# Performance work log

Hardware: AMD Instinct MI355X
Metric: run time of the kernel (lower is better)

The kernel has to match this reference:

```python
import jax, jax.numpy as jnp
import numpy as np

ALPHA = 0.2  # LeakyReLU negative slope
NUM_HEADS, OUT_DIM = 8, 16
N_NODES, N_EDGES, IN_DIM = 50000, 800000, 128


def setup_inputs() -> dict:
    key = jax.random.key(0)
    k = jax.random.split(key, 6)
    return {
        "x": jax.random.normal(k[0], (N_NODES, IN_DIM), dtype=jnp.float32),
        "W1": jax.random.normal(k[1], (IN_DIM, IN_DIM), dtype=jnp.float32) * (1.414 / np.sqrt(IN_DIM)),
        "W2": jax.random.normal(k[2], (NUM_HEADS * OUT_DIM, IN_DIM), dtype=jnp.float32) * (1.414 / np.sqrt(IN_DIM)),
        "attn_l": jax.random.normal(k[3], (NUM_HEADS, OUT_DIM), dtype=jnp.float32) * 0.3,
        "attn_r": jax.random.normal(k[4], (NUM_HEADS, OUT_DIM), dtype=jnp.float32) * 0.3,
        "edge_index": jax.random.randint(k[5], (2, N_EDGES), 0, N_NODES, dtype=jnp.int64),
    }


def reference(x, W1, W2, attn_l, attn_r, edge_index):
    N = x.shape[0]
    H, D = attn_l.shape
    # fc1 -> leaky_relu -> fc2, reshape to per-head features [N, H, D]
    h2 = jax.nn.leaky_relu(x @ W1.T, ALPHA)
    ft = (h2 @ W2.T).reshape(N, H, D)
    # per-node attention halves: a1 = ft . attn_l, a2 = ft . attn_r  -> [N, H]
    a1 = jnp.einsum('nhd,hd->nh', ft, attn_l)
    a2 = jnp.einsum('nhd,hd->nh', ft, attn_r)
    src, dst = edge_index[0], edge_index[1]
    # edge attention logits [E, H]
    e = jax.nn.leaky_relu(a1[src] + a2[dst], ALPHA)
    # edge softmax normalized over incoming edges of each dst node
    emax = jax.ops.segment_max(e, dst, num_segments=N)
    ee = jnp.exp(e - emax[dst])
    esum = jax.ops.segment_sum(ee, dst, num_segments=N)
    a = ee / esum[dst]  # [E, H]
    # weighted scatter-sum aggregation: sum_{e: dst(e)=n} a_e * ft[src(e)]
    msg = ft[src] * a[:, :, None]  # [E, H, D]
    out = jax.ops.segment_sum(msg, dst, num_segments=N)  # [N, H, D]
    return out
```

## Files before the change

kernel.cpp:

```cpp
#include <hip/hip_runtime.h>

#define ALPHA 0.2f
constexpr int N = 50000;
constexpr int E = 800000;

typedef __attribute__((ext_vector_type(8))) short bf16x8;
typedef __attribute__((ext_vector_type(4))) float f32x4;

__device__ inline ushort f2bf(float v) {
  uint u = __float_as_uint(v);
  return (ushort)((u + 0x7fff + ((u >> 16) & 1)) >> 16);
}
__device__ inline float bf2f(ushort u) { return __uint_as_float(((uint)u) << 16); }

constexpr int LDX = 136;

constexpr int BN   = 128;
constexpr int NB   = (N + BN - 1) / BN;
constexpr int NBP  = 512;
constexpr int PSTR = 392;
constexpr int CHUNK = 4096;
constexpr int NBLK  = (E + CHUNK - 1) / CHUNK;
constexpr int FEATB = (N + 63) / 64;

__global__ __launch_bounds__(256) void k1_kernel(const float* __restrict__ W1,
    const float* __restrict__ W2, ushort* __restrict__ wf1hi, ushort* __restrict__ wf1lo,
    ushort* __restrict__ wf2hi, ushort* __restrict__ wf2lo,
    const int* __restrict__ dst, int* __restrict__ partial) {
  const int bid = blockIdx.x;
  const int t = threadIdx.x;
  if (bid < NBLK) {
    __shared__ int lh[NB];
    const int e0 = bid * CHUNK, e1 = min(e0 + CHUNK, E);
    for (int i = t; i < NB; i += 256) lh[i] = 0;
    __syncthreads();
    for (int i = e0 + t; i < e1; i += 256)
      atomicAdd(&lh[((unsigned)dst[i]) >> 7], 1);
    __syncthreads();
    for (int i = t; i < NB; i += 256) partial[bid * PSTR + i] = lh[i];
    return;
  }
  int g = (bid - NBLK) * 256 + t;
  const float* W = (g < 2048) ? W1 : W2;
  ushort* whi = (g < 2048) ? wf1hi : wf2hi;
  ushort* wlo = (g < 2048) ? wf1lo : wf2lo;
  int f = g & 2047;
  int ks = f >> 9, rem = f & 511, jb = rem >> 6, l = rem & 63;
  int m = jb * 16 + (l & 15), kb = ks * 32 + (l >> 4) * 8;
#pragma unroll
  for (int q = 0; q < 2; ++q) {
    float4 v = *(const float4*)&W[m * 128 + kb + q * 4];
    ushort4 hi, lo;
    hi.x = f2bf(v.x); lo.x = f2bf(v.x - bf2f(hi.x));
    hi.y = f2bf(v.y); lo.y = f2bf(v.y - bf2f(hi.y));
    hi.z = f2bf(v.z); lo.z = f2bf(v.z - bf2f(hi.z));
    hi.w = f2bf(v.w); lo.w = f2bf(v.w - bf2f(hi.w));
    *(ushort4*)&whi[f * 8 + q * 4] = hi;
    *(ushort4*)&wlo[f * 8 + q * 4] = lo;
  }
}

__global__ __launch_bounds__(NBP) void colscan_kernel(const int* __restrict__ partial,
    int* __restrict__ bucket_base, int* __restrict__ chunk_base) {
  __shared__ int sh[NBP];
  const int t = threadIdx.x;
  int tot = 0;
  if (t < NB)
    for (int blk = 0; blk < NBLK; ++blk) tot += partial[blk * PSTR + t];
  sh[t] = (t < NB) ? tot : 0;
  __syncthreads();
  for (int off = 1; off < NBP; off <<= 1) {
    int u = (t >= off) ? sh[t - off] : 0;
    __syncthreads();
    sh[t] += u;
    __syncthreads();
  }
  if (t < NB) {
    int base = sh[t] - tot;
    bucket_base[t] = base;
    int run = base;
    for (int blk = 0; blk < NBLK; ++blk) {
      chunk_base[blk * PSTR + t] = run;
      run += partial[blk * PSTR + t];
    }
  }
  if (t == NB - 1) bucket_base[NB] = sh[t];
}

__global__ __launch_bounds__(256) void featpart_kernel(
    const float* __restrict__ x,
    const ushort* __restrict__ wf1hi, const ushort* __restrict__ wf1lo,
    const ushort* __restrict__ wf2hi, const ushort* __restrict__ wf2lo,
    const float* __restrict__ attn_l, const float* __restrict__ attn_r,
    ushort* __restrict__ ft_bf, float* __restrict__ a1, float* __restrict__ a2,
    const int* __restrict__ src, const int* __restrict__ dst,
    const int* __restrict__ partial, const int* __restrict__ chunk_base,
    int* __restrict__ ebuf) {
  extern __shared__ char smem[];
  const int bid = blockIdx.x;
  const int tid = threadIdx.x;

  if (bid < NBLK) {
    int* hist = (int*)smem;
    int* sA   = hist + NBP;
    int* sB   = sA + NBP;
    int* curs = sB + NBP;
    int* buf  = curs + NBP;
    const int e0 = bid * CHUNK, e1 = min(e0 + CHUNK, E);
    for (int k = tid; k < NBP; k += 256) {
      int h = (k < NB) ? partial[bid * PSTR + k] : 0;
      hist[k] = h;
      sA[k] = h;
    }
    __syncthreads();
    int* pin = sA; int* pout = sB;
    for (int off = 1; off < NBP; off <<= 1) {
      for (int k = tid; k < NBP; k += 256)
        pout[k] = pin[k] + ((k >= off) ? pin[k - off] : 0);
      __syncthreads();
      int* tmp = pin; pin = pout; pout = tmp;
    }
    for (int k = tid; k < NBP; k += 256) curs[k] = pin[k] - hist[k];
    __syncthreads();
    for (int i = e0 + tid; i < e1; i += 256) {
      int s = src[i], d = dst[i];
      int p = atomicAdd(&curs[((unsigned)d) >> 7], 1);
      buf[p] = (s << 7) | (d & 127);
    }
    __syncthreads();
    const int total = e1 - e0;
    for (int i = tid; i < total; i += 256) {
      int lo = 0, hi = NB;
      while (lo < hi) { int m = (lo + hi) >> 1; if (pin[m] > i) hi = m; else lo = m + 1; }
      int rank = i - (pin[lo] - hist[lo]);
      ebuf[chunk_base[bid * PSTR + lo] + rank] = buf[i];
    }
    return;
  }

  ushort* sXhi = (ushort*)smem;
  ushort* sXlo = sXhi + 64 * LDX;
  const int w = tid >> 6, l = tid & 63;
  const int lr = l & 15, lg4 = l >> 4;
  const int rowBase = (bid - NBLK) * 64;

  for (int i = tid; i < 64 * 32; i += 256) {
    int row = i >> 5, kc = i & 31;
    int g = rowBase + row;
    float4 v = make_float4(0.f, 0.f, 0.f, 0.f);
    if (g < N) v = reinterpret_cast<const float4*>(x)[g * 32 + kc];
    ushort4 hi, lo;
    hi.x = f2bf(v.x); lo.x = f2bf(v.x - bf2f(hi.x));
    hi.y = f2bf(v.y); lo.y = f2bf(v.y - bf2f(hi.y));
    hi.z = f2bf(v.z); lo.z = f2bf(v.z - bf2f(hi.z));
    hi.w = f2bf(v.w); lo.w = f2bf(v.w - bf2f(hi.w));
    *(ushort4*)&sXhi[row * LDX + kc * 4] = hi;
    *(ushort4*)&sXlo[row * LDX + kc * 4] = lo;
  }

  bf16x8 bh[4][2], bl[4][2];
#pragma unroll
  for (int ks = 0; ks < 4; ++ks)
#pragma unroll
    for (int jj = 0; jj < 2; ++jj) {
      int off = ((ks * 8 + (2 * w + jj)) * 64 + l) * 8;
      bh[ks][jj] = *(const bf16x8*)&wf1hi[off];
      bl[ks][jj] = *(const bf16x8*)&wf1lo[off];
    }
  __syncthreads();

  f32x4 acc[4][2];
#pragma unroll
  for (int mi = 0; mi < 4; ++mi)
#pragma unroll
    for (int jj = 0; jj < 2; ++jj) acc[mi][jj] = (f32x4){0.f, 0.f, 0.f, 0.f};

#pragma unroll
  for (int ks = 0; ks < 4; ++ks) {
    bf16x8 ah[4], al[4];
#pragma unroll
    for (int mi = 0; mi < 4; ++mi) {
      int addr = (mi * 16 + lr) * LDX + ks * 32 + lg4 * 8;
      ah[mi] = *(const bf16x8*)&sXhi[addr];
      al[mi] = *(const bf16x8*)&sXlo[addr];
    }
#pragma unroll
    for (int mi = 0; mi < 4; ++mi)
#pragma unroll
      for (int jj = 0; jj < 2; ++jj) {
        acc[mi][jj] = __builtin_amdgcn_mfma_f32_16x16x32_bf16(ah[mi], bh[ks][jj], acc[mi][jj], 0, 0, 0);
        acc[mi][jj] = __builtin_amdgcn_mfma_f32_16x16x32_bf16(ah[mi], bl[ks][jj], acc[mi][jj], 0, 0, 0);
        acc[mi][jj] = __builtin_amdgcn_mfma_f32_16x16x32_bf16(al[mi], bh[ks][jj], acc[mi][jj], 0, 0, 0);
      }
  }
  __syncthreads();

#pragma unroll
  for (int mi = 0; mi < 4; ++mi)
#pragma unroll
    for (int jj = 0; jj < 2; ++jj)
#pragma unroll
      for (int r = 0; r < 4; ++r) {
        float v = acc[mi][jj][r];
        v = v > 0.f ? v : ALPHA * v;
        int row = mi * 16 + lg4 * 4 + r;
        int col = w * 32 + jj * 16 + lr;
        ushort hv = f2bf(v);
        sXhi[row * LDX + col] = hv;
        sXlo[row * LDX + col] = f2bf(v - bf2f(hv));
      }
#pragma unroll
  for (int ks = 0; ks < 4; ++ks)
#pragma unroll
    for (int jj = 0; jj < 2; ++jj) {
      int off = ((ks * 8 + (2 * w + jj)) * 64 + l) * 8;
      bh[ks][jj] = *(const bf16x8*)&wf2hi[off];
      bl[ks][jj] = *(const bf16x8*)&wf2lo[off];
    }
  __syncthreads();

#pragma unroll
  for (int mi = 0; mi < 4; ++mi)
#pragma unroll
    for (int jj = 0; jj < 2; ++jj) acc[mi][jj] = (f32x4){0.f, 0.f, 0.f, 0.f};

#pragma unroll
  for (int ks = 0; ks < 4; ++ks) {
    bf16x8 ah[4], al[4];
#pragma unroll
    for (int mi = 0; mi < 4; ++mi) {
      int addr = (mi * 16 + lr) * LDX + ks * 32 + lg4 * 8;
      ah[mi] = *(const bf16x8*)&sXhi[addr];
      al[mi] = *(const bf16x8*)&sXlo[addr];
    }
#pragma unroll
    for (int mi = 0; mi < 4; ++mi)
#pragma unroll
      for (int jj = 0; jj < 2; ++jj) {
        acc[mi][jj] = __builtin_amdgcn_mfma_f32_16x16x32_bf16(ah[mi], bh[ks][jj], acc[mi][jj], 0, 0, 0);
        acc[mi][jj] = __builtin_amdgcn_mfma_f32_16x16x32_bf16(ah[mi], bl[ks][jj], acc[mi][jj], 0, 0, 0);
        acc[mi][jj] = __builtin_amdgcn_mfma_f32_16x16x32_bf16(al[mi], bh[ks][jj], acc[mi][jj], 0, 0, 0);
      }
  }

#pragma unroll
  for (int mi = 0; mi < 4; ++mi)
#pragma unroll
    for (int jj = 0; jj < 2; ++jj) {
      int h = 2 * w + jj;
      float alv = attn_l[h * 16 + lr], arv = attn_r[h * 16 + lr];
#pragma unroll
      for (int r = 0; r < 4; ++r) {
        float v = acc[mi][jj][r];
        int grow = rowBase + mi * 16 + lg4 * 4 + r;
        bool valid = grow < N;
        if (valid) ft_bf[grow * 128 + h * 16 + lr] = f2bf(v);
        float sl = v * alv, sr = v * arv;
#pragma unroll
        for (int off = 8; off; off >>= 1) {
          sl += __shfl_xor(sl, off, 16);
          sr += __shfl_xor(sr, off, 16);
        }
        if (valid && lr == 0) { a1[grow * 8 + h] = sl; a2[grow * 8 + h] = sr; }
      }
    }
}

__global__ __launch_bounds__(256) void fine_kernel(const int* __restrict__ ebuf,
    const int* __restrict__ bucket_base, int* __restrict__ row_ptr,
    int* __restrict__ col_src) {
  __shared__ int ldeg[BN], sc[BN], curs[BN];
  const int b = blockIdx.x, t = threadIdx.x;
  const int node0 = b * BN;
  const int nloc = min(BN, N - node0);
  const int bstart = bucket_base[b], bend = bucket_base[b + 1];
  if (t < BN) ldeg[t] = 0;
  __syncthreads();
  for (int i = bstart + t; i < bend; i += 256)
    atomicAdd(&ldeg[ebuf[i] & 127], 1);
  __syncthreads();
  if (t < BN) sc[t] = ldeg[t];
  __syncthreads();
#pragma unroll
  for (int off = 1; off < BN; off <<= 1) {
    int u = (t < BN && t >= off) ? sc[t - off] : 0;
    __syncthreads();
    if (t < BN) sc[t] += u;
    __syncthreads();
  }
  if (t < nloc) {
    int base = bstart + sc[t] - ldeg[t];
    row_ptr[node0 + t] = base;
    curs[t] = base;
  }
  if (b == NB - 1 && t == 0) row_ptr[N] = bend;
  __syncthreads();
  for (int i = bstart + t; i < bend; i += 256) {
    int pr = ebuf[i];
    int pos = atomicAdd(&curs[pr & 127], 1);
    col_src[pos] = pr >> 7;
  }
}

__global__ __launch_bounds__(256) void agg_kernel(const int* __restrict__ row_ptr,
    const int* __restrict__ col_src, const ushort* __restrict__ ft_bf,
    const float* __restrict__ a1, const float* __restrict__ a2,
    float* __restrict__ out) {
  const int node = blockIdx.x * 4 + (threadIdx.x >> 6);
  if (node >= N) return;
  const int t = threadIdx.x & 63;
  const int eSlot = t >> 3;
  const int hA = t & 7;
  const int hB = t >> 3;
  const int start = row_ptr[node], end = row_ptr[node + 1];
  const float a2nA = a2[node * 8 + hA];

  float l = 0.f, acc0 = 0.f, acc1 = 0.f;
  for (int base = start; base < end; base += 8) {
    int rem = end - base; rem = rem > 8 ? 8 : rem;
    int idx = base + (eSlot < rem ? eSlot : rem - 1);
    int s = col_src[idx];
    float lg = a1[s * 8 + hA] + a2nA;
    lg = lg > 0.f ? lg : ALPHA * lg;
    float p = (eSlot < rem) ? __expf(lg) : 0.f;
#pragma unroll
    for (int e = 0; e < 8; ++e) {
      float pe = __shfl(p, e * 8 + hB);
      int se = __shfl(s, e * 8);
      ushort2 f = *(const ushort2*)&ft_bf[se * 128 + t * 2];
      l += pe;
      acc0 = fmaf(pe, bf2f(f.x), acc0);
      acc1 = fmaf(pe, bf2f(f.y), acc1);
    }
  }
  float inv = (end > start) ? 1.f / l : 0.f;
  *(float2*)&out[node * 128 + t * 2] = make_float2(acc0 * inv, acc1 * inv);
}

extern "C" void kernel_launch(void* const* d_in, const int* in_sizes, int n_in,
                              void* d_out, int out_size, void* d_ws, size_t ws_size,
                              hipStream_t stream) {
  const float* x      = (const float*)d_in[0];
  const float* W1     = (const float*)d_in[1];
  const float* W2     = (const float*)d_in[2];
  const float* attn_l = (const float*)d_in[3];
  const float* attn_r = (const float*)d_in[4];
  const int*   edge   = (const int*)d_in[5];
  const int*   src    = edge;
  const int*   dst    = edge + E;
  float* out = (float*)d_out;

  char* ws = (char*)d_ws;
  ushort* ft_bf       = (ushort*)(ws);
  float*  a1          = (float*) (ws + 12800000);
  float*  a2          = (float*) (ws + 14400000);
  int*    row_ptr     = (int*)   (ws + 16000000);
  int*    bucket_base = (int*)   (ws + 16200064);
  int*    col_src     = (int*)   (ws + 16201664);
  ushort* wf1hi       = (ushort*)(ws + 19401664);
  ushort* wf1lo       = (ushort*)(ws + 19434432);
  ushort* wf2hi       = (ushort*)(ws + 19467200);
  ushort* wf2lo       = (ushort*)(ws + 19499968);
  int*    ebuf        = (int*)   (ws + 19532736);
  int*    partial     = (int*)   (ws + 22732736);
  int*    chunk_base  = (int*)   (ws + 23040064);

  k1_kernel<<<NBLK + 16, 256, 0, stream>>>(W1, W2, wf1hi, wf1lo, wf2hi, wf2lo, dst, partial);
  colscan_kernel<<<1, NBP, 0, stream>>>(partial, bucket_base, chunk_base);
  featpart_kernel<<<NBLK + FEATB, 256, 2 * 64 * LDX * sizeof(ushort), stream>>>(
      x, wf1hi, wf1lo, wf2hi, wf2lo, attn_l, attn_r, ft_bf, a1, a2,
      src, dst, partial, chunk_base, ebuf);
  fine_kernel<<<NB, 256, 0, stream>>>(ebuf, bucket_base, row_ptr, col_src);
  agg_kernel<<<(N + 3) / 4, 256, 0, stream>>>(row_ptr, col_src, ft_bf, a1, a2, out);
}
```

Before: 104.1 us.

## Shrink feature tiles to 32 rows and scatter edges directly via chunk cursors

```diff
diff --git a/kernel.cpp b/kernel.cpp
--- a/kernel.cpp
+++ b/kernel.cpp
@@ -21,7 +21,9 @@
 constexpr int PSTR = 392;
 constexpr int CHUNK = 4096;
 constexpr int NBLK  = (E + CHUNK - 1) / CHUNK;
-constexpr int FEATB = (N + 63) / 64;
+constexpr int FROWS = 32;
+constexpr int FEATB = (N + FROWS - 1) / FROWS;
+constexpr int SMEMB = 2 * FROWS * LDX * 2;
 
 __global__ __launch_bounds__(256) void k1_kernel(const float* __restrict__ W1,
     const float* __restrict__ W2, ushort* __restrict__ wf1hi, ushort* __restrict__ wf1lo,
@@ -87,64 +89,38 @@
   if (t == NB - 1) bucket_base[NB] = sh[t];
 }
 
-__global__ __launch_bounds__(256) void featpart_kernel(
+__global__ __launch_bounds__(256, 6) void featpart_kernel(
     const float* __restrict__ x,
     const ushort* __restrict__ wf1hi, const ushort* __restrict__ wf1lo,
     const ushort* __restrict__ wf2hi, const ushort* __restrict__ wf2lo,
     const float* __restrict__ attn_l, const float* __restrict__ attn_r,
     ushort* __restrict__ ft_bf, float* __restrict__ a1, float* __restrict__ a2,
     const int* __restrict__ src, const int* __restrict__ dst,
-    const int* __restrict__ partial, const int* __restrict__ chunk_base,
-    int* __restrict__ ebuf) {
+    const int* __restrict__ chunk_base, int* __restrict__ ebuf) {
   extern __shared__ char smem[];
   const int bid = blockIdx.x;
   const int tid = threadIdx.x;
 
   if (bid < NBLK) {
-    int* hist = (int*)smem;
-    int* sA   = hist + NBP;
-    int* sB   = sA + NBP;
-    int* curs = sB + NBP;
-    int* buf  = curs + NBP;
+    int* curs = (int*)smem;
     const int e0 = bid * CHUNK, e1 = min(e0 + CHUNK, E);
-    for (int k = tid; k < NBP; k += 256) {
-      int h = (k < NB) ? partial[bid * PSTR + k] : 0;
-      hist[k] = h;
-      sA[k] = h;
-    }
-    __syncthreads();
-    int* pin = sA; int* pout = sB;
-    for (int off = 1; off < NBP; off <<= 1) {
-      for (int k = tid; k < NBP; k += 256)
-        pout[k] = pin[k] + ((k >= off) ? pin[k - off] : 0);
-      __syncthreads();
-      int* tmp = pin; pin = pout; pout = tmp;
-    }
-    for (int k = tid; k < NBP; k += 256) curs[k] = pin[k] - hist[k];
+    for (int k = tid; k < NB; k += 256) curs[k] = chunk_base[bid * PSTR + k];
     __syncthreads();
     for (int i = e0 + tid; i < e1; i += 256) {
       int s = src[i], d = dst[i];
-      int p = atomicAdd(&curs[((unsigned)d) >> 7], 1);
-      buf[p] = (s << 7) | (d & 127);
-    }
-    __syncthreads();
-    const int total = e1 - e0;
-    for (int i = tid; i < total; i += 256) {
-      int lo = 0, hi = NB;
-      while (lo < hi) { int m = (lo + hi) >> 1; if (pin[m] > i) hi = m; else lo = m + 1; }
-      int rank = i - (pin[lo] - hist[lo]);
-      ebuf[chunk_base[bid * PSTR + lo] + rank] = buf[i];
+      int pos = atomicAdd(&curs[((unsigned)d) >> 7], 1);
+      ebuf[pos] = (s << 7) | (d & 127);
     }
     return;
   }
 
   ushort* sXhi = (ushort*)smem;
-  ushort* sXlo = sXhi + 64 * LDX;
+  ushort* sXlo = sXhi + FROWS * LDX;
   const int w = tid >> 6, l = tid & 63;
   const int lr = l & 15, lg4 = l >> 4;
-  const int rowBase = (bid - NBLK) * 64;
-
-  for (int i = tid; i < 64 * 32; i += 256) {
+  const int rowBase = (bid - NBLK) * FROWS;
+
+  for (int i = tid; i < FROWS * 32; i += 256) {
     int row = i >> 5, kc = i & 31;
     int g = rowBase + row;
     float4 v = make_float4(0.f, 0.f, 0.f, 0.f);
@@ -157,46 +133,42 @@
     *(ushort4*)&sXhi[row * LDX + kc * 4] = hi;
     *(ushort4*)&sXlo[row * LDX + kc * 4] = lo;
   }
-
-  bf16x8 bh[4][2], bl[4][2];
-#pragma unroll
-  for (int ks = 0; ks < 4; ++ks)
+  __syncthreads();
+
+  f32x4 acc[2][2];
+#pragma unroll
+  for (int mi = 0; mi < 2; ++mi)
+#pragma unroll
+    for (int jj = 0; jj < 2; ++jj) acc[mi][jj] = (f32x4){0.f, 0.f, 0.f, 0.f};
+
+#pragma unroll
+  for (int ks = 0; ks < 4; ++ks) {
+    bf16x8 bh[2], bl[2], ah[2], al[2];
 #pragma unroll
     for (int jj = 0; jj < 2; ++jj) {
       int off = ((ks * 8 + (2 * w + jj)) * 64 + l) * 8;
-      bh[ks][jj] = *(const bf16x8*)&wf1hi[off];
-      bl[ks][jj] = *(const bf16x8*)&wf1lo[off];
-    }
-  __syncthreads();
-
-  f32x4 acc[4][2];
-#pragma unroll
-  for (int mi = 0; mi < 4; ++mi)
-#pragma unroll
-    for (int jj = 0; jj < 2; ++jj) acc[mi][jj] = (f32x4){0.f, 0.f, 0.f, 0.f};
-
-#pragma unroll
-  for (int ks = 0; ks < 4; ++ks) {
-    bf16x8 ah[4], al[4];
-#pragma unroll
-    for (int mi = 0; mi < 4; ++mi) {
+      bh[jj] = *(const bf16x8*)&wf1hi[off];
+      bl[jj] = *(const bf16x8*)&wf1lo[off];
+    }
+#pragma unroll
+    for (int mi = 0; mi < 2; ++mi) {
       int addr = (mi * 16 + lr) * LDX + ks * 32 + lg4 * 8;
       ah[mi] = *(const bf16x8*)&sXhi[addr];
       al[mi] = *(const bf16x8*)&sXlo[addr];
     }
 #pragma unroll
-    for (int mi = 0; mi < 4; ++mi)
+    for (int mi = 0; mi < 2; ++mi)
 #pragma unroll
       for (int jj = 0; jj < 2; ++jj) {
-        acc[mi][jj] = __builtin_amdgcn_mfma_f32_16x16x32_bf16(ah[mi], bh[ks][jj], acc[mi][jj], 0, 0, 0);
-        acc[mi][jj] = __builtin_amdgcn_mfma_f32_16x16x32_bf16(ah[mi], bl[ks][jj], acc[mi][jj], 0, 0, 0);
-        acc[mi][jj] = __builtin_amdgcn_mfma_f32_16x16x32_bf16(al[mi], bh[ks][jj], acc[mi][jj], 0, 0, 0);
+        acc[mi][jj] = __builtin_amdgcn_mfma_f32_16x16x32_bf16(ah[mi], bh[jj], acc[mi][jj], 0, 0, 0);
+        acc[mi][jj] = __builtin_amdgcn_mfma_f32_16x16x32_bf16(ah[mi], bl[jj], acc[mi][jj], 0, 0, 0);
+        acc[mi][jj] = __builtin_amdgcn_mfma_f32_16x16x32_bf16(al[mi], bh[jj], acc[mi][jj], 0, 0, 0);
       }
   }
   __syncthreads();
 
 #pragma unroll
-  for (int mi = 0; mi < 4; ++mi)
+  for (int mi = 0; mi < 2; ++mi)
 #pragma unroll
     for (int jj = 0; jj < 2; ++jj)
 #pragma unroll
@@ -209,42 +181,40 @@
         sXhi[row * LDX + col] = hv;
         sXlo[row * LDX + col] = f2bf(v - bf2f(hv));
       }
-#pragma unroll
-  for (int ks = 0; ks < 4; ++ks)
+  __syncthreads();
+
+#pragma unroll
+  for (int mi = 0; mi < 2; ++mi)
+#pragma unroll
+    for (int jj = 0; jj < 2; ++jj) acc[mi][jj] = (f32x4){0.f, 0.f, 0.f, 0.f};
+
+#pragma unroll
+  for (int ks = 0; ks < 4; ++ks) {
+    bf16x8 bh[2], bl[2], ah[2], al[2];
 #pragma unroll
     for (int jj = 0; jj < 2; ++jj) {
       int off = ((ks * 8 + (2 * w + jj)) * 64 + l) * 8;
-      bh[ks][jj] = *(const bf16x8*)&wf2hi[off];
-      bl[ks][jj] = *(const bf16x8*)&wf2lo[off];
-    }
-  __syncthreads();
-
-#pragma unroll
-  for (int mi = 0; mi < 4; ++mi)
-#pragma unroll
-    for (int jj = 0; jj < 2; ++jj) acc[mi][jj] = (f32x4){0.f, 0.f, 0.f, 0.f};
-
-#pragma unroll
-  for (int ks = 0; ks < 4; ++ks) {
-    bf16x8 ah[4], al[4];
-#pragma unroll
-    for (int mi = 0; mi < 4; ++mi) {
+      bh[jj] = *(const bf16x8*)&wf2hi[off];
+      bl[jj] = *(const bf16x8*)&wf2lo[off];
+    }
+#pragma unroll
+    for (int mi = 0; mi < 2; ++mi) {
       int addr = (mi * 16 + lr) * LDX + ks * 32 + lg4 * 8;
       ah[mi] = *(const bf16x8*)&sXhi[addr];
       al[mi] = *(const bf16x8*)&sXlo[addr];
     }
 #pragma unroll
-    for (int mi = 0; mi < 4; ++mi)
+    for (int mi = 0; mi < 2; ++mi)
 #pragma unroll
       for (int jj = 0; jj < 2; ++jj) {
-        acc[mi][jj] = __builtin_amdgcn_mfma_f32_16x16x32_bf16(ah[mi], bh[ks][jj], acc[mi][jj], 0, 0, 0);
-        acc[mi][jj] = __builtin_amdgcn_mfma_f32_16x16x32_bf16(ah[mi], bl[ks][jj], acc[mi][jj], 0, 0, 0);
-        acc[mi][jj] = __builtin_amdgcn_mfma_f32_16x16x32_bf16(al[mi], bh[ks][jj], acc[mi][jj], 0, 0, 0);
+        acc[mi][jj] = __builtin_amdgcn_mfma_f32_16x16x32_bf16(ah[mi], bh[jj], acc[mi][jj], 0, 0, 0);
+        acc[mi][jj] = __builtin_amdgcn_mfma_f32_16x16x32_bf16(ah[mi], bl[jj], acc[mi][jj], 0, 0, 0);
+        acc[mi][jj] = __builtin_amdgcn_mfma_f32_16x16x32_bf16(al[mi], bh[jj], acc[mi][jj], 0, 0, 0);
       }
   }
 
 #pragma unroll
-  for (int mi = 0; mi < 4; ++mi)
+  for (int mi = 0; mi < 2; ++mi)
 #pragma unroll
     for (int jj = 0; jj < 2; ++jj) {
       int h = 2 * w + jj;
@@ -367,9 +337,9 @@
 
   k1_kernel<<<NBLK + 16, 256, 0, stream>>>(W1, W2, wf1hi, wf1lo, wf2hi, wf2lo, dst, partial);
   colscan_kernel<<<1, NBP, 0, stream>>>(partial, bucket_base, chunk_base);
-  featpart_kernel<<<NBLK + FEATB, 256, 2 * 64 * LDX * sizeof(ushort), stream>>>(
+  featpart_kernel<<<NBLK + FEATB, 256, SMEMB, stream>>>(
       x, wf1hi, wf1lo, wf2hi, wf2lo, attn_l, attn_r, ft_bf, a1, a2,
-      src, dst, partial, chunk_base, ebuf);
+      src, dst, chunk_base, ebuf);
   fine_kernel<<<NB, 256, 0, stream>>>(ebuf, bucket_base, row_ptr, col_src);
   agg_kernel<<<(N + 3) / 4, 256, 0, stream>>>(row_ptr, col_src, ft_bf, a1, a2, out);
 }
```

New measurement: 98.37 us, median of 2. 1.06x faster.
